# Kernel optimization log

Measured on AMD Instinct MI355X. Metric: run time of the kernel, lower is better.

The kernel has to match this reference:

```python
import jax, jax.numpy as jnp
import numpy as np

B, T, P, V, D, DINO, H, L = 32, 40, 256, 4096, 256, 384, 4, 2
HD = D // H          # head dim 64
DFF = 4 * D          # 1024
EPS = 1e-5


def setup_inputs() -> dict:
    key = jax.random.key(0)
    ks = iter(jax.random.split(key, 40))
    rn = lambda shape, s=0.02: jax.random.normal(next(ks), shape, jnp.float32) * s
    return dict(
        patches=jax.random.normal(next(ks), (B, P, DINO), jnp.float32),
        tokens=jax.random.randint(next(ks), (B, T), 0, V, jnp.int32),
        tok_emb=rn((V, D)),
        pos_emb=rn((1, T, D)),
        qkv_w=rn((L, 3 * D, D)), qkv_b=jnp.zeros((L, 3 * D), jnp.float32),
        out_w=rn((L, D, D)), out_b=jnp.zeros((L, D), jnp.float32),
        ln1_s=jnp.ones((L, D), jnp.float32), ln1_b=jnp.zeros((L, D), jnp.float32),
        w1=rn((L, DFF, D)), b1=jnp.zeros((L, DFF), jnp.float32),
        w2=rn((L, D, DFF)), b2=jnp.zeros((L, D), jnp.float32),
        ln2_s=jnp.ones((L, D), jnp.float32), ln2_b=jnp.zeros((L, D), jnp.float32),
        fus_w1=rn((D, DINO + D)), fus_b1=jnp.zeros((D,), jnp.float32),
        fus_w2=rn((D, D)), fus_b2=jnp.zeros((D,), jnp.float32),
        cls_w=rn((V, D)), cls_b=jnp.zeros((V,), jnp.float32),
    )


def _ln(x, s, b):
    m = jnp.mean(x, -1, keepdims=True)
    v = jnp.var(x, -1, keepdims=True)
    return (x - m) * jax.lax.rsqrt(v + EPS) * s + b


def _token_encoder(tokens, tok_emb, pos_emb, qkv_w, qkv_b, out_w, out_b,
                   ln1_s, ln1_b, w1, b1, w2, b2, ln2_s, ln2_b):
    # Causal full-sequence pass: output at position t equals re-running the
    # unmasked encoder on tokens[:, :t+1] and taking the last position.
    x = tok_emb[tokens] + pos_emb[:, :tokens.shape[1], :]   # [B,T,D]
    causal = jnp.triu(jnp.full((T, T), -1e9, jnp.float32), 1)  # [T,T]
    for l in range(L):  # fixed small layer count
        qkv = x @ qkv_w[l].T + qkv_b[l]                     # [B,T,3D]
        q, k, v = jnp.split(qkv, 3, axis=-1)
        q = q.reshape(B, T, H, HD).transpose(0, 2, 1, 3)    # [B,H,T,hd]
        k = k.reshape(B, T, H, HD).transpose(0, 2, 1, 3)
        v = v.reshape(B, T, H, HD).transpose(0, 2, 1, 3)
        scores = jnp.einsum('bhqd,bhkd->bhqk', q, k) / np.sqrt(HD).astype(np.float32)
        attn = jax.nn.softmax(scores + causal, axis=-1)
        ctx = jnp.einsum('bhqk,bhkd->bhqd', attn, v)        # [B,H,T,hd]
        ctx = ctx.transpose(0, 2, 1, 3).reshape(B, T, D)
        x = _ln(x + ctx @ out_w[l].T + out_b[l], ln1_s[l], ln1_b[l])
        h = jax.nn.relu(x @ w1[l].T + b1[l]) @ w2[l].T + b2[l]
        x = _ln(x + h, ln2_s[l], ln2_b[l])
    return x  # [B,T,D]


def reference(patches, tokens, tok_emb, pos_emb, qkv_w, qkv_b, out_w, out_b,
              ln1_s, ln1_b, w1, b1, w2, b2, ln2_s, ln2_b,
              fus_w1, fus_b1, fus_w2, fus_b2, cls_w, cls_b):
    enc = _token_encoder(tokens, tok_emb, pos_emb, qkv_w, qkv_b, out_w, out_b,
                         ln1_s, ln1_b, w1, b1, w2, b2, ln2_s, ln2_b)  # [B,T,D]
    # context for step 0 is zeros; step t>0 uses encoder output at position t-1
    ctx = jnp.concatenate([jnp.zeros((B, 1, D), enc.dtype), enc[:, :-1]], axis=1)  # [B,T,D]
    # fusion MLP: split the concat-linear into a patch part and a context part
    wp, wc = fus_w1[:, :DINO], fus_w1[:, DINO:]
    pproj = patches @ wp.T                                  # [B,P,D]
    cproj = ctx @ wc.T + fus_b1                             # [B,T,D]
    h = jax.nn.gelu(pproj[:, None, :, :] + cproj[:, :, None, :], approximate=False)  # [B,T,P,D]
    fused = h @ fus_w2.T + fus_b2                           # [B,T,P,D]
    # sigmoid+gather of the 4096-way logits == gather classifier rows, dot, sigmoid
    w_sel = cls_w[tokens]                                   # [B,T,D]
    b_sel = cls_b[tokens]                                   # [B,T]
    logits = jnp.einsum('btpd,btd->btp', fused, w_sel) + b_sel[:, :, None]
    probs = jax.nn.sigmoid(logits)                          # [B,T,P]
    return probs.transpose(0, 2, 1)                         # [B,P,T] == [B,256,40]
```

## Files before the change

kernel.cpp:

```cpp
#include <hip/hip_runtime.h>
#include <hip/hip_bf16.h>

#define B_ 32
#define T_ 40
#define P_ 256
#define V_ 4096
#define D_ 256
#define DINO_ 384
#define H_ 4
#define L_ 2
#define HD_ 64
#define DFF_ 1024
#define EPS_ 1e-5f

typedef __bf16 bf16;
typedef __bf16 bf16x8 __attribute__((ext_vector_type(8)));
typedef float f32x4 __attribute__((ext_vector_type(4)));

#define OFF_QKV 0
#define OFF_OUTW 393216
#define OFF_W1 524288
#define OFF_W2 1048576
#define OFF_FUS 1572864
#define WB_TOTAL 1736704
#define CONV_BLOCKS 848
#define PAT_BLOCKS 1536
#define PREP_UNITS 3728

__device__ __forceinline__ bf16x8 cvt8(const float* p) {
  float4 f0 = *(const float4*)p;
  float4 f1 = *(const float4*)(p + 4);
  bf16x8 v;
  v[0] = (bf16)f0.x; v[1] = (bf16)f0.y; v[2] = (bf16)f0.z; v[3] = (bf16)f0.w;
  v[4] = (bf16)f1.x; v[5] = (bf16)f1.y; v[6] = (bf16)f1.z; v[7] = (bf16)f1.w;
  return v;
}

struct GemmSM  { bf16 As[32 * 72];  bf16 Ws[32 * 72]; };
struct CprojSM { bf16 As[32 * 264]; bf16 Ws[32 * 72]; };
struct AttnSM  { float q[20][65]; float k[40][65]; float v[40][65]; float s[20][41]; };
struct PrepSM  { float tile[32][33]; };
struct FinalSM { float2 cws[4][D_]; };
struct RowSM   { bf16 As[32 * 72];  bf16 Ws[256 * 72]; };

struct Params {
  const float* patches; const int* tokens; const float* tok_emb; const float* pos_emb;
  const float* qkv_w; const float* qkv_b; const float* out_w; const float* out_b;
  const float* ln1_s; const float* ln1_b; const float* w1; const float* b1;
  const float* w2; const float* b2; const float* ln2_s; const float* ln2_b;
  const float* fus_w1; const float* fus_b1; const float* fus_w2; const float* fus_b2;
  const float* cls_w; const float* cls_b; float* out;
  float* x; float* qkvbuf; float* attbuf; float* s; float* pprojT; float* cw;
  bf16* wb; bf16* w2Tb; bf16* patb; bf16* hb;
};

template <int ABF16, int OBF16, int RELU, int RESID, int GATH, int CW>
__device__ __forceinline__ void tile_gemm(
    bf16* As, bf16* Ws, const void* Av, const bf16* W, const float* bias,
    const float* resid, const int* tokens, void* outv, int K, int lda,
    int ldw, int ldc, int bm, int bn) {
  const int tid = threadIdx.x;
  const int lane = tid & 63;
  const int wv = tid >> 6;
  const int mi = wv & 1, ni = wv >> 1;
  const int col = lane & 15, quad = lane >> 4;
  const int srow = tid >> 3, kc = (tid & 7) * 8;
  const float* Af = (const float*)Av;
  const bf16* Ab = (const bf16*)Av;
  const float* Ag = GATH ? (Af + (long)tokens[bm + srow] * D_) : nullptr;
  const bf16* Wp = W + (long)(bn + srow) * ldw + kc;

  f32x4 acc = {0.f, 0.f, 0.f, 0.f};
  for (int kk = 0; kk < K; kk += 64) {
    if (GATH)
      *(bf16x8*)&As[srow * 72 + kc] = cvt8(Ag + kk + kc);
    else if (ABF16)
      *(bf16x8*)&As[srow * 72 + kc] = *(const bf16x8*)(Ab + (long)(bm + srow) * lda + kk + kc);
    else
      *(bf16x8*)&As[srow * 72 + kc] = cvt8(Af + (long)(bm + srow) * lda + kk + kc);
    *(bf16x8*)&Ws[srow * 72 + kc] = *(const bf16x8*)(Wp + kk);
    __syncthreads();
#pragma unroll
    for (int ki = 0; ki < 2; ++ki) {
      bf16x8 afr = *(const bf16x8*)&As[(mi * 16 + col) * 72 + ki * 32 + quad * 8];
      bf16x8 bfr = *(const bf16x8*)&Ws[(ni * 16 + col) * 72 + ki * 32 + quad * 8];
      acc = __builtin_amdgcn_mfma_f32_16x16x32_bf16(afr, bfr, acc, 0, 0, 0);
    }
    __syncthreads();
  }
  const int n = bn + ni * 16 + col;
  float bv = bias ? bias[n] : 0.0f;
#pragma unroll
  for (int r = 0; r < 4; ++r) {
    int m = bm + mi * 16 + quad * 4 + r;
    float val = acc[r] + bv;
    if (RESID) val += resid[(long)m * D_ + n];
    if (RELU) val = fmaxf(val, 0.0f);
    if (CW == 1) ((float*)outv)[(long)m * (2 * D_) + n * 2] = val;
    else if (CW == 2) ((float*)outv)[(long)m * (2 * D_) + n * 2 + 1] = val;
    else if (OBF16) ((bf16*)outv)[(long)m * ldc + n] = (bf16)val;
    else ((float*)outv)[(long)m * ldc + n] = val;
  }
}

__device__ __forceinline__ void do_prep(PrepSM& ps, const Params& P, int u) {
  int tid = threadIdx.x;
  if (u < 1280) {
    P.x[u * D_ + tid] = P.tok_emb[(long)P.tokens[u] * D_ + tid] + P.pos_emb[(u % T_) * D_ + tid];
  } else if (u < 1344) {
    int tt = u - 1280;
    int bx = (tt & 7) * 32, by = (tt >> 3) * 32;
    int tx = tid & 31, ty = tid >> 5;
#pragma unroll
    for (int i = 0; i < 32; i += 8) ps.tile[ty + i][tx] = P.fus_w2[(by + ty + i) * D_ + bx + tx];
    __syncthreads();
#pragma unroll
    for (int i = 0; i < 32; i += 8)
      P.w2Tb[(bx + ty + i) * D_ + by + tx] = (bf16)ps.tile[tx][ty + i];
  } else if (u < 1344 + CONV_BLOCKS) {
    long f = (long)(u - 1344) * 2048 + tid * 8;
    const float* src; long off;
    if (f < OFF_OUTW)      { src = P.qkv_w;  off = f; }
    else if (f < OFF_W1)   { src = P.out_w;  off = f - OFF_OUTW; }
    else if (f < OFF_W2)   { src = P.w1;     off = f - OFF_W1; }
    else if (f < OFF_FUS)  { src = P.w2;     off = f - OFF_W2; }
    else                   { src = P.fus_w1; off = f - OFF_FUS; }
    *(bf16x8*)&P.wb[f] = cvt8(src + off);
  } else {
    long f = (long)(u - 1344 - CONV_BLOCKS) * 2048 + tid * 8;
    *(bf16x8*)&P.patb[f] = cvt8(P.patches + f);
  }
}

__device__ __forceinline__ void do_qkv(GemmSM& g, const Params& P, int l, int u) {
  tile_gemm<0, 0, 0, 0, 0, 0>(g.As, g.Ws, P.x, P.wb + OFF_QKV + (long)l * 3 * D_ * D_,
                              P.qkv_b + l * 3 * D_, nullptr, nullptr, P.qkvbuf,
                              256, D_, D_, 3 * D_, (u / 24) * 32, (u % 24) * 32);
}
__device__ __forceinline__ void do_w1(GemmSM& g, const Params& P, int l, int u) {
  tile_gemm<0, 1, 1, 0, 0, 0>(g.As, g.Ws, P.x, P.wb + OFF_W1 + (long)l * DFF_ * D_,
                              P.b1 + l * DFF_, nullptr, nullptr, P.hb,
                              256, D_, D_, DFF_, (u / 32) * 32, (u % 32) * 32);
}
__device__ __forceinline__ void do_w2(GemmSM& g, const Params& P, int l, int u) {
  tile_gemm<1, 0, 0, 1, 0, 0>(g.As, g.Ws, P.hb, P.wb + OFF_W2 + (long)l * D_ * DFF_,
                              P.b2 + l * D_, P.x, nullptr, P.s,
                              DFF_, DFF_, DFF_, D_, (u / 8) * 32, (u % 8) * 32);
}
__device__ __forceinline__ void do_pproj(GemmSM& g, const Params& P, int t) {
  int bn = (t & 7) * 32; int y = t >> 3; int bb = y >> 3; int bm = (y & 7) * 32;
  tile_gemm<1, 0, 0, 0, 0, 0>(g.As, g.Ws, P.wb + OFF_FUS, P.patb + (long)bb * P_ * DINO_,
                              nullptr, nullptr, nullptr, P.pprojT + (long)bb * D_ * P_,
                              384, 640, DINO_, P_, bm, bn);
}
__device__ __forceinline__ void do_weff(GemmSM& g, const Params& P, int t) {
  tile_gemm<0, 0, 0, 0, 1, 2>(g.As, g.Ws, P.cls_w, P.w2Tb, nullptr, nullptr,
                              P.tokens, P.cw, 256, D_, D_, D_,
                              (t / 8) * 32, (t % 8) * 32);
}

__device__ __forceinline__ void do_attn(AttnSM& A, const Params& P, int u) {
  int h = u & 3, b = (u >> 2) & 31, zq = u >> 7;
  int r0 = zq * 20;
  int tid = threadIdx.x;
  int lane = tid & 63, wv = tid >> 6;
  const float* qkv = P.qkvbuf;
  for (int idx = tid; idx < T_ * HD_; idx += 256) {
    int t = idx >> 6, d = idx & 63;
    long base = (long)(b * T_ + t) * (3 * D_) + h * HD_ + d;
    A.k[t][d] = qkv[base + D_];
    A.v[t][d] = qkv[base + 2 * D_];
    if (t < 20) A.q[t][d] = qkv[(long)(b * T_ + r0 + t) * (3 * D_) + h * HD_ + d];
  }
  __syncthreads();
  for (int idx = tid; idx < 20 * T_; idx += 256) {
    int i = idx / T_, j = idx - i * T_;
    if (j <= r0 + i) {
      float acc = 0.f;
#pragma unroll
      for (int d = 0; d < HD_; ++d) acc += A.q[i][d] * A.k[j][d];
      A.s[i][j] = acc * 0.125f;
    }
  }
  __syncthreads();
  for (int rr = wv; rr < 20; rr += 4) {
    int hi = r0 + rr;
    float val = (lane <= hi) ? A.s[rr][lane] : -1e30f;
    float mx = val;
#pragma unroll
    for (int mk = 1; mk < 64; mk <<= 1) mx = fmaxf(mx, __shfl_xor(mx, mk));
    float e = (lane <= hi)
                  ? __builtin_amdgcn_exp2f((val - mx) * 1.4426950408889634f)
                  : 0.f;
    float sum = e;
#pragma unroll
    for (int mk = 1; mk < 64; mk <<= 1) sum += __shfl_xor(sum, mk);
    float inv = __builtin_amdgcn_rcpf(sum);
    if (lane < T_) A.s[rr][lane] = e * inv;
  }
  __syncthreads();
  for (int idx = tid; idx < 20 * HD_; idx += 256) {
    int i = idx >> 6, d = idx & 63;
    int hi = r0 + i;
    float acc = 0.f;
    for (int j = 0; j <= hi; ++j) acc += A.s[i][j] * A.v[j][d];
    P.attbuf[(long)(b * T_ + hi) * D_ + h * HD_ + d] = acc;
  }
}

__device__ __forceinline__ void do_cproj(CprojSM& c, const Params& P, int bm, int bn) {
  const int tid = threadIdx.x;
  const int lane = tid & 63;
  const int wv = tid >> 6;
  const int mi = wv & 1, ni = wv >> 1;
  const int col = lane & 15, quad = lane >> 4;
  const int srow = tid >> 3, kc = (tid & 7) * 8;
  const int gm = bm + srow;
  f32x4 acc = {0.f, 0.f, 0.f, 0.f};
  const int cg = (tid & 7) * 32;
  const int t = gm % T_;
  if (t == 0) {
    bf16x8 z8 = {};
#pragma unroll
    for (int i = 0; i < 4; ++i) *(bf16x8*)&c.As[srow * 264 + cg + i * 8] = z8;
  } else {
    const float* sp = P.s + (long)(gm - 1) * D_ + cg;
    float v[32];
    float sum = 0.f, ss = 0.f;
#pragma unroll
    for (int i = 0; i < 8; ++i) {
      float4 f = *(const float4*)(sp + i * 4);
      v[i*4] = f.x; v[i*4+1] = f.y; v[i*4+2] = f.z; v[i*4+3] = f.w;
      sum += f.x + f.y + f.z + f.w;
      ss += f.x*f.x + f.y*f.y + f.z*f.z + f.w*f.w;
    }
#pragma unroll
    for (int mk = 1; mk < 8; mk <<= 1) {
      sum += __shfl_xor(sum, mk);
      ss += __shfl_xor(ss, mk);
    }
    float mean = sum * (1.0f / D_);
    float inv = rsqrtf(ss * (1.0f / D_) - mean * mean + EPS_);
    const float* lng = P.ln2_s + D_;
    const float* lnb = P.ln2_b + D_;
#pragma unroll
    for (int i = 0; i < 8; ++i) {
      float4 g4 = *(const float4*)(lng + cg + i * 4);
      float4 b4 = *(const float4*)(lnb + cg + i * 4);
      c.As[srow*264 + cg + i*4]     = (bf16)((v[i*4]   - mean) * inv * g4.x + b4.x);
      c.As[srow*264 + cg + i*4 + 1] = (bf16)((v[i*4+1] - mean) * inv * g4.y + b4.y);
      c.As[srow*264 + cg + i*4 + 2] = (bf16)((v[i*4+2] - mean) * inv * g4.z + b4.z);
      c.As[srow*264 + cg + i*4 + 3] = (bf16)((v[i*4+3] - mean) * inv * g4.w + b4.w);
    }
  }
  __syncthreads();
  const bf16* Wp = P.wb + OFF_FUS + 384 + (long)(bn + srow) * 640 + kc;
  for (int kk = 0; kk < 256; kk += 64) {
    *(bf16x8*)&c.Ws[srow * 72 + kc] = *(const bf16x8*)(Wp + kk);
    __syncthreads();
#pragma unroll
    for (int ki = 0; ki < 2; ++ki) {
      bf16x8 afr = *(const bf16x8*)&c.As[(mi*16 + col) * 264 + kk + ki*32 + quad*8];
      bf16x8 bfr = *(const bf16x8*)&c.Ws[(ni*16 + col) * 72 + ki*32 + quad*8];
      acc = __builtin_amdgcn_mfma_f32_16x16x32_bf16(afr, bfr, acc, 0, 0, 0);
    }
    __syncthreads();
  }
  const int n = bn + ni * 16 + col;
  float bv = P.fus_b1[n];
#pragma unroll
  for (int r = 0; r < 4; ++r) {
    int m = bm + mi * 16 + quad * 4 + r;
    P.cw[(long)m * (2 * D_) + n * 2] = acc[r] + bv;
  }
}

__device__ __forceinline__ void do_final(FinalSM& F, const Params& P, int u) {
  int tid = threadIdx.x;
  int lane = tid & 63, wv = tid >> 6;
  int px = u & 3, rest = u >> 2;
  int ty = rest % 10, b = rest / 10;
  int p = px * 64 + lane;
  int t = ty * 4 + wv;
  int mbase = b * T_ + ty * 4;
  for (int idx = tid; idx < 4 * D_; idx += 256) {
    int tt = idx >> 8, e = idx & 255;
    F.cws[tt][e] = ((const float2*)P.cw)[(long)(mbase + tt) * D_ + e];
  }
  __syncthreads();

  int m = b * T_ + t;
  int tok = P.tokens[m];
  const float* cr = P.cls_w + (long)tok * D_;
  float bacc = 0.f;
#pragma unroll
  for (int i = 0; i < 4; ++i) bacc += cr[lane + i * 64] * P.fus_b2[lane + i * 64];
#pragma unroll
  for (int mk = 1; mk < 64; mk <<= 1) bacc += __shfl_xor(bacc, mk);
  float beff = bacc + P.cls_b[tok];

  const float* ppb = P.pprojT + (long)b * (D_ * P_);
  float acc = 0.f;
#pragma unroll 8
  for (int e = 0; e < D_; ++e) {
    float pp = ppb[e * P_ + p];
    float2 c = F.cws[wv][e];
    float x = pp + c.x;
    float ex = __builtin_amdgcn_exp2f(-2.4554248f * x);
    float r = __builtin_amdgcn_rcpf(1.0f + ex);
    acc = fmaf(x * r, c.y, acc);
  }
  float logit = acc + beff;
  float es = __builtin_amdgcn_exp2f(-1.4426950408889634f * logit);
  P.out[(long)(b * P_ + p) * T_ + t] = __builtin_amdgcn_rcpf(1.0f + es);
}

template <int ABF16>
__global__ __launch_bounds__(256) void rowln_k(
    const void* __restrict__ Av, const bf16* __restrict__ W,
    const float* __restrict__ bias, const float* __restrict__ resid,
    const float* __restrict__ lng, const float* __restrict__ lnb,
    float* __restrict__ xout, int K, int lda, int ldw) {
  __shared__ RowSM sm;
  const int tid = threadIdx.x;
  const int lane = tid & 63;
  const int wv = tid >> 6;
  const int mi = wv & 1, nh = wv >> 1;
  const int col = lane & 15, quad = lane >> 4;
  const int srow = tid >> 3, kc = (tid & 7) * 8;
  const int bm = blockIdx.x * 32;
  const float* Af = (const float*)Av;
  const bf16* Ab = (const bf16*)Av;

  f32x4 acc[8];
#pragma unroll
  for (int i = 0; i < 8; ++i) acc[i] = (f32x4){0.f, 0.f, 0.f, 0.f};

  for (int kk = 0; kk < K; kk += 64) {
    if (ABF16)
      *(bf16x8*)&sm.As[srow * 72 + kc] =
          *(const bf16x8*)(Ab + (long)(bm + srow) * lda + kk + kc);
    else
      *(bf16x8*)&sm.As[srow * 72 + kc] = cvt8(Af + (long)(bm + srow) * lda + kk + kc);
    {
      const bf16* wp = W + (long)tid * ldw + kk;
#pragma unroll
      for (int j = 0; j < 8; ++j)
        *(bf16x8*)&sm.Ws[tid * 72 + j * 8] = *(const bf16x8*)(wp + j * 8);
    }
    __syncthreads();
#pragma unroll
    for (int nn = 0; nn < 8; ++nn) {
      const int ni = nh * 8 + nn;
#pragma unroll
      for (int ki = 0; ki < 2; ++ki) {
        bf16x8 afr = *(const bf16x8*)&sm.As[(mi * 16 + col) * 72 + ki * 32 + quad * 8];
        bf16x8 bfr = *(const bf16x8*)&sm.Ws[(ni * 16 + col) * 72 + ki * 32 + quad * 8];
        acc[nn] = __builtin_amdgcn_mfma_f32_16x16x32_bf16(afr, bfr, acc[nn], 0, 0, 0);
      }
    }
    __syncthreads();
  }

  float* S = (float*)sm.Ws;
#pragma unroll
  for (int nn = 0; nn < 8; ++nn) {
    const int n = (nh * 8 + nn) * 16 + col;
    const float bv = bias[n];
#pragma unroll
    for (int r = 0; r < 4; ++r) {
      const int m = mi * 16 + quad * 4 + r;
      S[m * 260 + n] = acc[nn][r] + bv + resid[(long)(bm + m) * D_ + n];
    }
  }
  __syncthreads();
  {
    const int row = tid >> 3, cg = (tid & 7) * 32;
    float v[32];
    float sum = 0.f, ss = 0.f;
#pragma unroll
    for (int i = 0; i < 8; ++i) {
      float4 f = *(const float4*)&S[row * 260 + cg + i * 4];
      v[i*4] = f.x; v[i*4+1] = f.y; v[i*4+2] = f.z; v[i*4+3] = f.w;
      sum += f.x + f.y + f.z + f.w;
      ss += f.x*f.x + f.y*f.y + f.z*f.z + f.w*f.w;
    }
#pragma unroll
    for (int mk = 1; mk < 8; mk <<= 1) {
      sum += __shfl_xor(sum, mk);
      ss += __shfl_xor(ss, mk);
    }
    const float mean = sum * (1.0f / D_);
    const float inv = rsqrtf(ss * (1.0f / D_) - mean * mean + EPS_);
#pragma unroll
    for (int i = 0; i < 8; ++i) {
      float4 g4 = *(const float4*)(lng + cg + i * 4);
      float4 b4 = *(const float4*)(lnb + cg + i * 4);
      float4 o;
      o.x = (v[i*4]   - mean) * inv * g4.x + b4.x;
      o.y = (v[i*4+1] - mean) * inv * g4.y + b4.y;
      o.z = (v[i*4+2] - mean) * inv * g4.z + b4.z;
      o.w = (v[i*4+3] - mean) * inv * g4.w + b4.w;
      *(float4*)(xout + (long)(bm + row) * D_ + cg + i * 4) = o;
    }
  }
}

__global__ __launch_bounds__(256) void prep_k(Params P) {
  __shared__ PrepSM ps; do_prep(ps, P, blockIdx.x);
}
__global__ __launch_bounds__(256) void qkv_k(Params P, int l) {
  __shared__ GemmSM g; do_qkv(g, P, l, blockIdx.x);
}
__global__ __launch_bounds__(256) void apw_k(Params P) {
  __shared__ union __align__(16) { AttnSM a; GemmSM g; } sm;
  int bid = blockIdx.x;
  if (bid < 256) do_attn(sm.a, P, bid);
  else if (bid < 2304) do_pproj(sm.g, P, bid - 256);
  else do_weff(sm.g, P, bid - 2304);
}
__global__ __launch_bounds__(256) void attn_k(Params P) {
  __shared__ AttnSM a; do_attn(a, P, blockIdx.x);
}
__global__ __launch_bounds__(256) void w1_k(Params P, int l) {
  __shared__ GemmSM g; do_w1(g, P, l, blockIdx.x);
}
__global__ __launch_bounds__(256) void w2_k(Params P, int l) {
  __shared__ GemmSM g; do_w2(g, P, l, blockIdx.x);
}
__global__ __launch_bounds__(256) void cproj_k(Params P) {
  __shared__ CprojSM c; do_cproj(c, P, blockIdx.y * 32, blockIdx.x * 32);
}
__global__ __launch_bounds__(256) void final_k(Params P) {
  __shared__ FinalSM f; do_final(f, P, blockIdx.x);
}

extern "C" void kernel_launch(void* const* d_in, const int* in_sizes, int n_in, void* d_out,
                              int out_size, void* d_ws, size_t ws_size, hipStream_t stream) {
  Params P;
  P.patches = (const float*)d_in[0];
  P.tokens = (const int*)d_in[1];
  P.tok_emb = (const float*)d_in[2];
  P.pos_emb = (const float*)d_in[3];
  P.qkv_w = (const float*)d_in[4];
  P.qkv_b = (const float*)d_in[5];
  P.out_w = (const float*)d_in[6];
  P.out_b = (const float*)d_in[7];
  P.ln1_s = (const float*)d_in[8];
  P.ln1_b = (const float*)d_in[9];
  P.w1 = (const float*)d_in[10];
  P.b1 = (const float*)d_in[11];
  P.w2 = (const float*)d_in[12];
  P.b2 = (const float*)d_in[13];
  P.ln2_s = (const float*)d_in[14];
  P.ln2_b = (const float*)d_in[15];
  P.fus_w1 = (const float*)d_in[16];
  P.fus_b1 = (const float*)d_in[17];
  P.fus_w2 = (const float*)d_in[18];
  P.fus_b2 = (const float*)d_in[19];
  P.cls_w = (const float*)d_in[20];
  P.cls_b = (const float*)d_in[21];
  P.out = (float*)d_out;

  const int MT = B_ * T_;
  P.x = (float*)d_ws;
  P.qkvbuf = P.x + MT * D_;
  P.attbuf = P.qkvbuf + MT * 3 * D_;
  P.s = P.attbuf + MT * D_;
  P.pprojT = P.s + MT * D_;
  P.cw = P.pprojT + (long)B_ * D_ * P_;
  P.wb = (bf16*)(P.cw + MT * D_ * 2);
  P.w2Tb = P.wb + WB_TOTAL;
  P.patb = P.w2Tb + D_ * D_;
  P.hb = P.patb + (long)B_ * P_ * DINO_;

  prep_k<<<PREP_UNITS, 256, 0, stream>>>(P);
  qkv_k<<<960, 256, 0, stream>>>(P, 0);
  apw_k<<<2624, 256, 0, stream>>>(P);
  rowln_k<0><<<40, 256, 0, stream>>>(P.attbuf, P.wb + OFF_OUTW, P.out_b, P.x,
                                     P.ln1_s, P.ln1_b, P.x, 256, 256, 256);
  w1_k<<<1280, 256, 0, stream>>>(P, 0);
  rowln_k<1><<<40, 256, 0, stream>>>(P.hb, P.wb + OFF_W2, P.b2, P.x,
                                     P.ln2_s, P.ln2_b, P.x, 1024, 1024, 1024);
  qkv_k<<<960, 256, 0, stream>>>(P, 1);
  attn_k<<<256, 256, 0, stream>>>(P);
  rowln_k<0><<<40, 256, 0, stream>>>(P.attbuf, P.wb + OFF_OUTW + D_ * D_,
                                     P.out_b + D_, P.x, P.ln1_s + D_,
                                     P.ln1_b + D_, P.x, 256, 256, 256);
  w1_k<<<1280, 256, 0, stream>>>(P, 1);
  w2_k<<<320, 256, 0, stream>>>(P, 1);
  cproj_k<<<dim3(8, 40), 256, 0, stream>>>(P);
  final_k<<<1280, 256, 0, stream>>>(P);
}
```

Before: 267.3 us.

## Fuse attention, out-proj+LN, and FFN+LN into one per-layer kernel

Replaces the separate attention, out-projection+LayerNorm, W1 and W2+LayerNorm launches with one layer kernel. Each of 80 blocks handles 16 rows end to end, keeping attention context, the hidden activations and the residual in shared memory. The pproj and weff work is split across the two layer kernels as extra blocks so it runs alongside the layer blocks. This removes several launches and global round-trips for the hidden activations. The cost is that only 80 blocks do the heavy FFN work, each streaming every layer weight, so parallelism is lower and weight traffic repeats across blocks.

```diff
diff --git a/kernel.cpp b/kernel.cpp
--- a/kernel.cpp
+++ b/kernel.cpp
@@ -38,10 +38,16 @@
 
 struct GemmSM  { bf16 As[32 * 72];  bf16 Ws[32 * 72]; };
 struct CprojSM { bf16 As[32 * 264]; bf16 Ws[32 * 72]; };
-struct AttnSM  { float q[20][65]; float k[40][65]; float v[40][65]; float s[20][41]; };
 struct PrepSM  { float tile[32][33]; };
 struct FinalSM { float2 cws[4][D_]; };
-struct RowSM   { bf16 As[32 * 72];  bf16 Ws[256 * 72]; };
+struct __align__(16) LayerSM {
+  bf16 CP[16 * 264];
+  union {
+    struct { float KS[80 * 68]; float VS[80 * 68]; float QS[16 * 68]; float SS[16 * 64]; } at;
+    struct { bf16 Ws[256 * 72]; float S1[16 * 260]; bf16 HB[16 * 136]; } gm;
+  } u;
+};
+union __align__(16) LayerU { LayerSM L; GemmSM g; };
 
 struct Params {
   const float* patches; const int* tokens; const float* tok_emb; const float* pos_emb;
@@ -137,16 +143,6 @@
                               P.qkv_b + l * 3 * D_, nullptr, nullptr, P.qkvbuf,
                               256, D_, D_, 3 * D_, (u / 24) * 32, (u % 24) * 32);
 }
-__device__ __forceinline__ void do_w1(GemmSM& g, const Params& P, int l, int u) {
-  tile_gemm<0, 1, 1, 0, 0, 0>(g.As, g.Ws, P.x, P.wb + OFF_W1 + (long)l * DFF_ * D_,
-                              P.b1 + l * DFF_, nullptr, nullptr, P.hb,
-                              256, D_, D_, DFF_, (u / 32) * 32, (u % 32) * 32);
-}
-__device__ __forceinline__ void do_w2(GemmSM& g, const Params& P, int l, int u) {
-  tile_gemm<1, 0, 0, 1, 0, 0>(g.As, g.Ws, P.hb, P.wb + OFF_W2 + (long)l * D_ * DFF_,
-                              P.b2 + l * D_, P.x, nullptr, P.s,
-                              DFF_, DFF_, DFF_, D_, (u / 8) * 32, (u % 8) * 32);
-}
 __device__ __forceinline__ void do_pproj(GemmSM& g, const Params& P, int t) {
   int bn = (t & 7) * 32; int y = t >> 3; int bb = y >> 3; int bm = (y & 7) * 32;
   tile_gemm<1, 0, 0, 0, 0, 0>(g.As, g.Ws, P.wb + OFF_FUS, P.patb + (long)bb * P_ * DINO_,
@@ -157,55 +153,6 @@
   tile_gemm<0, 0, 0, 0, 1, 2>(g.As, g.Ws, P.cls_w, P.w2Tb, nullptr, nullptr,
                               P.tokens, P.cw, 256, D_, D_, D_,
                               (t / 8) * 32, (t % 8) * 32);
-}
-
-__device__ __forceinline__ void do_attn(AttnSM& A, const Params& P, int u) {
-  int h = u & 3, b = (u >> 2) & 31, zq = u >> 7;
-  int r0 = zq * 20;
-  int tid = threadIdx.x;
-  int lane = tid & 63, wv = tid >> 6;
-  const float* qkv = P.qkvbuf;
-  for (int idx = tid; idx < T_ * HD_; idx += 256) {
-    int t = idx >> 6, d = idx & 63;
-    long base = (long)(b * T_ + t) * (3 * D_) + h * HD_ + d;
-    A.k[t][d] = qkv[base + D_];
-    A.v[t][d] = qkv[base + 2 * D_];
-    if (t < 20) A.q[t][d] = qkv[(long)(b * T_ + r0 + t) * (3 * D_) + h * HD_ + d];
-  }
-  __syncthreads();
-  for (int idx = tid; idx < 20 * T_; idx += 256) {
-    int i = idx / T_, j = idx - i * T_;
-    if (j <= r0 + i) {
-      float acc = 0.f;
-#pragma unroll
-      for (int d = 0; d < HD_; ++d) acc += A.q[i][d] * A.k[j][d];
-      A.s[i][j] = acc * 0.125f;
-    }
-  }
-  __syncthreads();
-  for (int rr = wv; rr < 20; rr += 4) {
-    int hi = r0 + rr;
-    float val = (lane <= hi) ? A.s[rr][lane] : -1e30f;
-    float mx = val;
-#pragma unroll
-    for (int mk = 1; mk < 64; mk <<= 1) mx = fmaxf(mx, __shfl_xor(mx, mk));
-    float e = (lane <= hi)
-                  ? __builtin_amdgcn_exp2f((val - mx) * 1.4426950408889634f)
-                  : 0.f;
-    float sum = e;
-#pragma unroll
-    for (int mk = 1; mk < 64; mk <<= 1) sum += __shfl_xor(sum, mk);
-    float inv = __builtin_amdgcn_rcpf(sum);
-    if (lane < T_) A.s[rr][lane] = e * inv;
-  }
-  __syncthreads();
-  for (int idx = tid; idx < 20 * HD_; idx += 256) {
-    int i = idx >> 6, d = idx & 63;
-    int hi = r0 + i;
-    float acc = 0.f;
-    for (int j = 0; j <= hi; ++j) acc += A.s[i][j] * A.v[j][d];
-    P.attbuf[(long)(b * T_ + hi) * D_ + h * HD_ + d] = acc;
-  }
 }
 
 __device__ __forceinline__ void do_cproj(CprojSM& c, const Params& P, int bm, int bn) {
@@ -315,93 +262,258 @@
   P.out[(long)(b * P_ + p) * T_ + t] = __builtin_amdgcn_rcpf(1.0f + es);
 }
 
-template <int ABF16>
-__global__ __launch_bounds__(256) void rowln_k(
-    const void* __restrict__ Av, const bf16* __restrict__ W,
-    const float* __restrict__ bias, const float* __restrict__ resid,
-    const float* __restrict__ lng, const float* __restrict__ lnb,
-    float* __restrict__ xout, int K, int lda, int ldw) {
-  __shared__ RowSM sm;
+template <int LAYER>
+__global__ __launch_bounds__(256) void layer_k(Params P) {
+  __shared__ LayerU sm;
+  const int bid = blockIdx.x;
+  if (bid >= 80) {
+    int t = bid - 80 + (LAYER == 0 ? 0 : 1024);
+    if (t < 2048) do_pproj(sm.g, P, t);
+    else do_weff(sm.g, P, t - 2048);
+    return;
+  }
   const int tid = threadIdx.x;
   const int lane = tid & 63;
   const int wv = tid >> 6;
-  const int mi = wv & 1, nh = wv >> 1;
   const int col = lane & 15, quad = lane >> 4;
-  const int srow = tid >> 3, kc = (tid & 7) * 8;
-  const int bm = blockIdx.x * 32;
-  const float* Af = (const float*)Av;
-  const bf16* Ab = (const bf16*)Av;
-
-  f32x4 acc[8];
-#pragma unroll
-  for (int i = 0; i < 8; ++i) acc[i] = (f32x4){0.f, 0.f, 0.f, 0.f};
-
-  for (int kk = 0; kk < K; kk += 64) {
-    if (ABF16)
-      *(bf16x8*)&sm.As[srow * 72 + kc] =
-          *(const bf16x8*)(Ab + (long)(bm + srow) * lda + kk + kc);
-    else
-      *(bf16x8*)&sm.As[srow * 72 + kc] = cvt8(Af + (long)(bm + srow) * lda + kk + kc);
-    {
-      const bf16* wp = W + (long)tid * ldw + kk;
-#pragma unroll
-      for (int j = 0; j < 8; ++j)
-        *(bf16x8*)&sm.Ws[tid * 72 + j * 8] = *(const bf16x8*)(wp + j * 8);
-    }
-    __syncthreads();
-#pragma unroll
-    for (int nn = 0; nn < 8; ++nn) {
-      const int ni = nh * 8 + nn;
+  const int R0 = bid * 16;
+  const int b_lo = R0 / T_, b_hi = (R0 + 15) / T_;
+  const int base = b_lo * T_, nr = (b_hi - b_lo + 1) * T_;
+
+  {
+    auto& A = sm.L.u.at;
+    for (int h = 0; h < H_; ++h) {
+      for (int idx = tid; idx < nr * 64; idx += 256) {
+        int t = idx >> 6, d = idx & 63;
+        long qb = (long)(base + t) * (3 * D_) + h * HD_ + d;
+        A.KS[t * 68 + d] = P.qkvbuf[qb + D_];
+        A.VS[t * 68 + d] = P.qkvbuf[qb + 2 * D_];
+      }
+      for (int idx = tid; idx < 16 * 64; idx += 256) {
+        int i = idx >> 6, d = idx & 63;
+        A.QS[i * 68 + d] = P.qkvbuf[(long)(R0 + i) * (3 * D_) + h * HD_ + d];
+      }
+      __syncthreads();
+      for (int idx = tid; idx < 16 * T_; idx += 256) {
+        int i = idx / T_, j = idx - i * T_;
+        int gr = R0 + i, ti = gr % T_;
+        if (j <= ti) {
+          int kr = (gr / T_) * T_ - base + j;
+          float acc = 0.f;
+#pragma unroll
+          for (int d = 0; d < 64; ++d) acc += A.QS[i * 68 + d] * A.KS[kr * 68 + d];
+          A.SS[i * 64 + j] = acc * 0.125f;
+        }
+      }
+      __syncthreads();
+      for (int rr = wv; rr < 16; rr += 4) {
+        int ti = (R0 + rr) % T_;
+        float val = (lane <= ti) ? A.SS[rr * 64 + lane] : -1e30f;
+        float mx = val;
+#pragma unroll
+        for (int mk = 1; mk < 64; mk <<= 1) mx = fmaxf(mx, __shfl_xor(mx, mk));
+        float e = (lane <= ti)
+                      ? __builtin_amdgcn_exp2f((val - mx) * 1.4426950408889634f)
+                      : 0.f;
+        float sum = e;
+#pragma unroll
+        for (int mk = 1; mk < 64; mk <<= 1) sum += __shfl_xor(sum, mk);
+        float inv = __builtin_amdgcn_rcpf(sum);
+        if (lane < T_) A.SS[rr * 64 + lane] = e * inv;
+      }
+      __syncthreads();
+      for (int idx = tid; idx < 16 * 64; idx += 256) {
+        int i = idx >> 6, d = idx & 63;
+        int gr = R0 + i, ti = gr % T_;
+        int koff = (gr / T_) * T_ - base;
+        float acc = 0.f;
+        for (int j = 0; j <= ti; ++j) acc += A.SS[i * 64 + j] * A.VS[(koff + j) * 68 + d];
+        sm.L.CP[i * 264 + h * HD_ + d] = (bf16)acc;
+      }
+      __syncthreads();
+    }
+  }
+
+  auto& G = sm.L.u.gm;
+  const bf16* Wout = P.wb + OFF_OUTW + (long)LAYER * D_ * D_;
+  f32x4 accp[4];
+#pragma unroll
+  for (int i = 0; i < 4; ++i) accp[i] = (f32x4){0.f, 0.f, 0.f, 0.f};
+  for (int kc = 0; kc < 4; ++kc) {
+    const bf16* wp = Wout + (long)tid * D_ + kc * 64;
+#pragma unroll
+    for (int j = 0; j < 8; ++j)
+      *(bf16x8*)&G.Ws[tid * 72 + j * 8] = *(const bf16x8*)(wp + j * 8);
+    __syncthreads();
+#pragma unroll
+    for (int t = 0; t < 4; ++t) {
+      int ni = wv * 4 + t;
 #pragma unroll
       for (int ki = 0; ki < 2; ++ki) {
-        bf16x8 afr = *(const bf16x8*)&sm.As[(mi * 16 + col) * 72 + ki * 32 + quad * 8];
-        bf16x8 bfr = *(const bf16x8*)&sm.Ws[(ni * 16 + col) * 72 + ki * 32 + quad * 8];
-        acc[nn] = __builtin_amdgcn_mfma_f32_16x16x32_bf16(afr, bfr, acc[nn], 0, 0, 0);
-      }
-    }
-    __syncthreads();
-  }
-
-  float* S = (float*)sm.Ws;
-#pragma unroll
-  for (int nn = 0; nn < 8; ++nn) {
-    const int n = (nh * 8 + nn) * 16 + col;
-    const float bv = bias[n];
-#pragma unroll
-    for (int r = 0; r < 4; ++r) {
-      const int m = mi * 16 + quad * 4 + r;
-      S[m * 260 + n] = acc[nn][r] + bv + resid[(long)(bm + m) * D_ + n];
+        bf16x8 afr = *(const bf16x8*)&sm.L.CP[col * 264 + kc * 64 + ki * 32 + quad * 8];
+        bf16x8 bfr = *(const bf16x8*)&G.Ws[(ni * 16 + col) * 72 + ki * 32 + quad * 8];
+        accp[t] = __builtin_amdgcn_mfma_f32_16x16x32_bf16(afr, bfr, accp[t], 0, 0, 0);
+      }
+    }
+    __syncthreads();
+  }
+  {
+    const float* outb = P.out_b + LAYER * D_;
+#pragma unroll
+    for (int t = 0; t < 4; ++t) {
+      int n = (wv * 4 + t) * 16 + col;
+#pragma unroll
+      for (int r = 0; r < 4; ++r) {
+        int m = quad * 4 + r;
+        G.S1[m * 260 + n] = accp[t][r] + outb[n] + P.x[(long)(R0 + m) * D_ + n];
+      }
     }
   }
   __syncthreads();
-  {
-    const int row = tid >> 3, cg = (tid & 7) * 32;
+
+  if (tid < 128) {
+    int row = tid >> 3, cg = (tid & 7) * 32;
     float v[32];
     float sum = 0.f, ss = 0.f;
 #pragma unroll
-    for (int i = 0; i < 8; ++i) {
-      float4 f = *(const float4*)&S[row * 260 + cg + i * 4];
-      v[i*4] = f.x; v[i*4+1] = f.y; v[i*4+2] = f.z; v[i*4+3] = f.w;
-      sum += f.x + f.y + f.z + f.w;
-      ss += f.x*f.x + f.y*f.y + f.z*f.z + f.w*f.w;
+    for (int i = 0; i < 32; ++i) {
+      float f = G.S1[row * 260 + cg + i];
+      v[i] = f; sum += f; ss += f * f;
     }
 #pragma unroll
     for (int mk = 1; mk < 8; mk <<= 1) {
       sum += __shfl_xor(sum, mk);
       ss += __shfl_xor(ss, mk);
     }
-    const float mean = sum * (1.0f / D_);
-    const float inv = rsqrtf(ss * (1.0f / D_) - mean * mean + EPS_);
-#pragma unroll
-    for (int i = 0; i < 8; ++i) {
-      float4 g4 = *(const float4*)(lng + cg + i * 4);
-      float4 b4 = *(const float4*)(lnb + cg + i * 4);
-      float4 o;
-      o.x = (v[i*4]   - mean) * inv * g4.x + b4.x;
-      o.y = (v[i*4+1] - mean) * inv * g4.y + b4.y;
-      o.z = (v[i*4+2] - mean) * inv * g4.z + b4.z;
-      o.w = (v[i*4+3] - mean) * inv * g4.w + b4.w;
-      *(float4*)(xout + (long)(bm + row) * D_ + cg + i * 4) = o;
+    float mean = sum * (1.0f / D_);
+    float inv = rsqrtf(ss * (1.0f / D_) - mean * mean + EPS_);
+    const float* lg = P.ln1_s + LAYER * D_;
+    const float* lb = P.ln1_b + LAYER * D_;
+#pragma unroll
+    for (int i = 0; i < 32; ++i) {
+      float o = (v[i] - mean) * inv * lg[cg + i] + lb[cg + i];
+      G.S1[row * 260 + cg + i] = o;
+      sm.L.CP[row * 264 + cg + i] = (bf16)o;
+    }
+  }
+  __syncthreads();
+
+  const bf16* W1 = P.wb + OFF_W1 + (long)LAYER * DFF_ * D_;
+  const bf16* W2 = P.wb + OFF_W2 + (long)LAYER * D_ * DFF_;
+  const float* b1l = P.b1 + LAYER * DFF_;
+  f32x4 acc2[4];
+#pragma unroll
+  for (int i = 0; i < 4; ++i) acc2[i] = (f32x4){0.f, 0.f, 0.f, 0.f};
+  for (int kk2 = 0; kk2 < 8; ++kk2) {
+    f32x4 acch[2];
+    acch[0] = (f32x4){0.f, 0.f, 0.f, 0.f};
+    acch[1] = (f32x4){0.f, 0.f, 0.f, 0.f};
+    for (int kc = 0; kc < 4; ++kc) {
+      const bf16* wp = W1 + (long)(kk2 * 128 + (tid >> 1)) * D_ + kc * 64 + (tid & 1) * 32;
+#pragma unroll
+      for (int j = 0; j < 4; ++j)
+        *(bf16x8*)&G.Ws[(tid >> 1) * 72 + (tid & 1) * 32 + j * 8] = *(const bf16x8*)(wp + j * 8);
+      __syncthreads();
+#pragma unroll
+      for (int t2 = 0; t2 < 2; ++t2) {
+        int ni = wv * 2 + t2;
+#pragma unroll
+        for (int ki = 0; ki < 2; ++ki) {
+          bf16x8 afr = *(const bf16x8*)&sm.L.CP[col * 264 + kc * 64 + ki * 32 + quad * 8];
+          bf16x8 bfr = *(const bf16x8*)&G.Ws[(ni * 16 + col) * 72 + ki * 32 + quad * 8];
+          acch[t2] = __builtin_amdgcn_mfma_f32_16x16x32_bf16(afr, bfr, acch[t2], 0, 0, 0);
+        }
+      }
+      __syncthreads();
+    }
+#pragma unroll
+    for (int t2 = 0; t2 < 2; ++t2) {
+      int n2 = (wv * 2 + t2) * 16 + col;
+#pragma unroll
+      for (int r = 0; r < 4; ++r) {
+        int m = quad * 4 + r;
+        float hv = fmaxf(acch[t2][r] + b1l[kk2 * 128 + n2], 0.f);
+        G.HB[m * 136 + n2] = (bf16)hv;
+      }
+    }
+    __syncthreads();
+    for (int sc = 0; sc < 2; ++sc) {
+      const bf16* wp = W2 + (long)tid * DFF_ + kk2 * 128 + sc * 64;
+#pragma unroll
+      for (int j = 0; j < 8; ++j)
+        *(bf16x8*)&G.Ws[tid * 72 + j * 8] = *(const bf16x8*)(wp + j * 8);
+      __syncthreads();
+#pragma unroll
+      for (int t = 0; t < 4; ++t) {
+        int ni = wv * 4 + t;
+#pragma unroll
+        for (int ki = 0; ki < 2; ++ki) {
+          bf16x8 afr = *(const bf16x8*)&G.HB[col * 136 + sc * 64 + ki * 32 + quad * 8];
+          bf16x8 bfr = *(const bf16x8*)&G.Ws[(ni * 16 + col) * 72 + ki * 32 + quad * 8];
+          acc2[t] = __builtin_amdgcn_mfma_f32_16x16x32_bf16(afr, bfr, acc2[t], 0, 0, 0);
+        }
+      }
+      __syncthreads();
+    }
+  }
+
+  {
+    const float* b2l = P.b2 + LAYER * D_;
+    float vals[4][4];
+#pragma unroll
+    for (int t = 0; t < 4; ++t) {
+      int n = (wv * 4 + t) * 16 + col;
+#pragma unroll
+      for (int r = 0; r < 4; ++r) {
+        int m = quad * 4 + r;
+        vals[t][r] = acc2[t][r] + b2l[n] + G.S1[m * 260 + n];
+      }
+    }
+    if (LAYER == 1) {
+#pragma unroll
+      for (int t = 0; t < 4; ++t) {
+        int n = (wv * 4 + t) * 16 + col;
+#pragma unroll
+        for (int r = 0; r < 4; ++r) {
+          int m = quad * 4 + r;
+          P.s[(long)(R0 + m) * D_ + n] = vals[t][r];
+        }
+      }
+    } else {
+#pragma unroll
+      for (int t = 0; t < 4; ++t) {
+        int n = (wv * 4 + t) * 16 + col;
+#pragma unroll
+        for (int r = 0; r < 4; ++r) {
+          int m = quad * 4 + r;
+          G.S1[m * 260 + n] = vals[t][r];
+        }
+      }
+      __syncthreads();
+      if (tid < 128) {
+        int row = tid >> 3, cg = (tid & 7) * 32;
+        float v[32];
+        float sum = 0.f, ss = 0.f;
+#pragma unroll
+        for (int i = 0; i < 32; ++i) {
+          float f = G.S1[row * 260 + cg + i];
+          v[i] = f; sum += f; ss += f * f;
+        }
+#pragma unroll
+        for (int mk = 1; mk < 8; mk <<= 1) {
+          sum += __shfl_xor(sum, mk);
+          ss += __shfl_xor(ss, mk);
+        }
+        float mean = sum * (1.0f / D_);
+        float inv = rsqrtf(ss * (1.0f / D_) - mean * mean + EPS_);
+        const float* lg = P.ln2_s;
+        const float* lb = P.ln2_b;
+#pragma unroll
+        for (int i = 0; i < 32; ++i) {
+          float o = (v[i] - mean) * inv * lg[cg + i] + lb[cg + i];
+          P.x[(long)(R0 + row) * D_ + cg + i] = o;
+        }
+      }
     }
   }
 }
@@ -412,24 +524,8 @@
 __global__ __launch_bounds__(256) void qkv_k(Params P, int l) {
   __shared__ GemmSM g; do_qkv(g, P, l, blockIdx.x);
 }
-__global__ __launch_bounds__(256) void apw_k(Params P) {
-  __shared__ union __align__(16) { AttnSM a; GemmSM g; } sm;
-  int bid = blockIdx.x;
-  if (bid < 256) do_attn(sm.a, P, bid);
-  else if (bid < 2304) do_pproj(sm.g, P, bid - 256);
-  else do_weff(sm.g, P, bid - 2304);
-}
-__global__ __launch_bounds__(256) void attn_k(Params P) {
-  __shared__ AttnSM a; do_attn(a, P, blockIdx.x);
-}
-__global__ __launch_bounds__(256) void w1_k(Params P, int l) {
-  __shared__ GemmSM g; do_w1(g, P, l, blockIdx.x);
-}
-__global__ __launch_bounds__(256) void w2_k(Params P, int l) {
-  __shared__ GemmSM g; do_w2(g, P, l, blockIdx.x);
-}
 __global__ __launch_bounds__(256) void cproj_k(Params P) {
-  __shared__ CprojSM c; do_cproj(c, P, blockIdx.y * 32, blockIdx.x * 32);
+  __shared__ CprojSM c; do_cproj(c, P, (blockIdx.x >> 3) * 32, (blockIdx.x & 7) * 32);
 }
 __global__ __launch_bounds__(256) void final_k(Params P) {
   __shared__ FinalSM f; do_final(f, P, blockIdx.x);
@@ -476,19 +572,9 @@
 
   prep_k<<<PREP_UNITS, 256, 0, stream>>>(P);
   qkv_k<<<960, 256, 0, stream>>>(P, 0);
-  apw_k<<<2624, 256, 0, stream>>>(P);
-  rowln_k<0><<<40, 256, 0, stream>>>(P.attbuf, P.wb + OFF_OUTW, P.out_b, P.x,
-                                     P.ln1_s, P.ln1_b, P.x, 256, 256, 256);
-  w1_k<<<1280, 256, 0, stream>>>(P, 0);
-  rowln_k<1><<<40, 256, 0, stream>>>(P.hb, P.wb + OFF_W2, P.b2, P.x,
-                                     P.ln2_s, P.ln2_b, P.x, 1024, 1024, 1024);
+  layer_k<0><<<80 + 1024, 256, 0, stream>>>(P);
   qkv_k<<<960, 256, 0, stream>>>(P, 1);
-  attn_k<<<256, 256, 0, stream>>>(P);
-  rowln_k<0><<<40, 256, 0, stream>>>(P.attbuf, P.wb + OFF_OUTW + D_ * D_,
-                                     P.out_b + D_, P.x, P.ln1_s + D_,
-                                     P.ln1_b + D_, P.x, 256, 256, 256);
-  w1_k<<<1280, 256, 0, stream>>>(P, 1);
-  w2_k<<<320, 256, 0, stream>>>(P, 1);
-  cproj_k<<<dim3(8, 40), 256, 0, stream>>>(P);
+  layer_k<1><<<80 + 1024 + 320, 256, 0, stream>>>(P);
+  cproj_k<<<320, 256, 0, stream>>>(P);
   final_k<<<1280, 256, 0, stream>>>(P);
 }
```

After: 343.8 us. 1.29x slower.

## Read fp32 weights directly in GEMMs and split fused row-LN into GEMM plus LN

Applied to the files above, without the earlier changes.

The prep kernel no longer converts the encoder weights (qkv, out, w1, w2) to bf16. The GEMM tile loader now converts fp32 weights on the fly, which removes a full pre-pass over about 1.5M weights. The fused 40-block row GEMM+LayerNorm kernels are replaced by a 320-block tiled projection GEMM that writes a residual sum, followed by a separate warp-per-row LayerNorm kernel. This gives more parallelism at the cost of extra launches and a round trip through global memory. The w2 GEMM of layer 0 is also restored as its own launch.

```diff
diff --git a/kernel.cpp b/kernel.cpp
--- a/kernel.cpp
+++ b/kernel.cpp
@@ -17,15 +17,10 @@
 typedef __bf16 bf16x8 __attribute__((ext_vector_type(8)));
 typedef float f32x4 __attribute__((ext_vector_type(4)));
 
-#define OFF_QKV 0
-#define OFF_OUTW 393216
-#define OFF_W1 524288
-#define OFF_W2 1048576
-#define OFF_FUS 1572864
-#define WB_TOTAL 1736704
-#define CONV_BLOCKS 848
+#define FUS_ELEMS 163840
+#define FUS_BLOCKS 80
 #define PAT_BLOCKS 1536
-#define PREP_UNITS 3728
+#define PREP_UNITS 2960
 
 __device__ __forceinline__ bf16x8 cvt8(const float* p) {
   float4 f0 = *(const float4*)p;
@@ -41,7 +36,6 @@
 struct AttnSM  { float q[20][65]; float k[40][65]; float v[40][65]; float s[20][41]; };
 struct PrepSM  { float tile[32][33]; };
 struct FinalSM { float2 cws[4][D_]; };
-struct RowSM   { bf16 As[32 * 72];  bf16 Ws[256 * 72]; };
 
 struct Params {
   const float* patches; const int* tokens; const float* tok_emb; const float* pos_emb;
@@ -54,9 +48,9 @@
   bf16* wb; bf16* w2Tb; bf16* patb; bf16* hb;
 };
 
-template <int ABF16, int OBF16, int RELU, int RESID, int GATH, int CW>
+template <int ABF16, int WF32, int OBF16, int RELU, int RESID, int GATH, int CW>
 __device__ __forceinline__ void tile_gemm(
-    bf16* As, bf16* Ws, const void* Av, const bf16* W, const float* bias,
+    bf16* As, bf16* Ws, const void* Av, const void* Wv, const float* bias,
     const float* resid, const int* tokens, void* outv, int K, int lda,
     int ldw, int ldc, int bm, int bn) {
   const int tid = threadIdx.x;
@@ -68,7 +62,8 @@
   const float* Af = (const float*)Av;
   const bf16* Ab = (const bf16*)Av;
   const float* Ag = GATH ? (Af + (long)tokens[bm + srow] * D_) : nullptr;
-  const bf16* Wp = W + (long)(bn + srow) * ldw + kc;
+  const float* Wpf = (const float*)Wv + (long)(bn + srow) * ldw + kc;
+  const bf16* Wpb = (const bf16*)Wv + (long)(bn + srow) * ldw + kc;
 
   f32x4 acc = {0.f, 0.f, 0.f, 0.f};
   for (int kk = 0; kk < K; kk += 64) {
@@ -78,7 +73,10 @@
       *(bf16x8*)&As[srow * 72 + kc] = *(const bf16x8*)(Ab + (long)(bm + srow) * lda + kk + kc);
     else
       *(bf16x8*)&As[srow * 72 + kc] = cvt8(Af + (long)(bm + srow) * lda + kk + kc);
-    *(bf16x8*)&Ws[srow * 72 + kc] = *(const bf16x8*)(Wp + kk);
+    if (WF32)
+      *(bf16x8*)&Ws[srow * 72 + kc] = cvt8(Wpf + kk);
+    else
+      *(bf16x8*)&Ws[srow * 72 + kc] = *(const bf16x8*)(Wpb + kk);
     __syncthreads();
 #pragma unroll
     for (int ki = 0; ki < 2; ++ki) {
@@ -117,46 +115,45 @@
 #pragma unroll
     for (int i = 0; i < 32; i += 8)
       P.w2Tb[(bx + ty + i) * D_ + by + tx] = (bf16)ps.tile[tx][ty + i];
-  } else if (u < 1344 + CONV_BLOCKS) {
+  } else if (u < 1344 + FUS_BLOCKS) {
     long f = (long)(u - 1344) * 2048 + tid * 8;
-    const float* src; long off;
-    if (f < OFF_OUTW)      { src = P.qkv_w;  off = f; }
-    else if (f < OFF_W1)   { src = P.out_w;  off = f - OFF_OUTW; }
-    else if (f < OFF_W2)   { src = P.w1;     off = f - OFF_W1; }
-    else if (f < OFF_FUS)  { src = P.w2;     off = f - OFF_W2; }
-    else                   { src = P.fus_w1; off = f - OFF_FUS; }
-    *(bf16x8*)&P.wb[f] = cvt8(src + off);
+    *(bf16x8*)&P.wb[f] = cvt8(P.fus_w1 + f);
   } else {
-    long f = (long)(u - 1344 - CONV_BLOCKS) * 2048 + tid * 8;
+    long f = (long)(u - 1344 - FUS_BLOCKS) * 2048 + tid * 8;
     *(bf16x8*)&P.patb[f] = cvt8(P.patches + f);
   }
 }
 
 __device__ __forceinline__ void do_qkv(GemmSM& g, const Params& P, int l, int u) {
-  tile_gemm<0, 0, 0, 0, 0, 0>(g.As, g.Ws, P.x, P.wb + OFF_QKV + (long)l * 3 * D_ * D_,
-                              P.qkv_b + l * 3 * D_, nullptr, nullptr, P.qkvbuf,
-                              256, D_, D_, 3 * D_, (u / 24) * 32, (u % 24) * 32);
+  tile_gemm<0, 1, 0, 0, 0, 0, 0>(g.As, g.Ws, P.x, P.qkv_w + (long)l * 3 * D_ * D_,
+                                 P.qkv_b + l * 3 * D_, nullptr, nullptr, P.qkvbuf,
+                                 256, D_, D_, 3 * D_, (u / 24) * 32, (u % 24) * 32);
+}
+__device__ __forceinline__ void do_proj(GemmSM& g, const Params& P, int l, int u) {
+  tile_gemm<0, 1, 0, 0, 1, 0, 0>(g.As, g.Ws, P.attbuf, P.out_w + (long)l * D_ * D_,
+                                 P.out_b + l * D_, P.x, nullptr, P.s,
+                                 256, D_, D_, D_, (u / 8) * 32, (u % 8) * 32);
 }
 __device__ __forceinline__ void do_w1(GemmSM& g, const Params& P, int l, int u) {
-  tile_gemm<0, 1, 1, 0, 0, 0>(g.As, g.Ws, P.x, P.wb + OFF_W1 + (long)l * DFF_ * D_,
-                              P.b1 + l * DFF_, nullptr, nullptr, P.hb,
-                              256, D_, D_, DFF_, (u / 32) * 32, (u % 32) * 32);
+  tile_gemm<0, 1, 1, 1, 0, 0, 0>(g.As, g.Ws, P.x, P.w1 + (long)l * DFF_ * D_,
+                                 P.b1 + l * DFF_, nullptr, nullptr, P.hb,
+                                 256, D_, D_, DFF_, (u / 32) * 32, (u % 32) * 32);
 }
 __device__ __forceinline__ void do_w2(GemmSM& g, const Params& P, int l, int u) {
-  tile_gemm<1, 0, 0, 1, 0, 0>(g.As, g.Ws, P.hb, P.wb + OFF_W2 + (long)l * D_ * DFF_,
-                              P.b2 + l * D_, P.x, nullptr, P.s,
-                              DFF_, DFF_, DFF_, D_, (u / 8) * 32, (u % 8) * 32);
+  tile_gemm<1, 1, 0, 0, 1, 0, 0>(g.As, g.Ws, P.hb, P.w2 + (long)l * D_ * DFF_,
+                                 P.b2 + l * D_, P.x, nullptr, P.s,
+                                 DFF_, DFF_, DFF_, D_, (u / 8) * 32, (u % 8) * 32);
 }
 __device__ __forceinline__ void do_pproj(GemmSM& g, const Params& P, int t) {
   int bn = (t & 7) * 32; int y = t >> 3; int bb = y >> 3; int bm = (y & 7) * 32;
-  tile_gemm<1, 0, 0, 0, 0, 0>(g.As, g.Ws, P.wb + OFF_FUS, P.patb + (long)bb * P_ * DINO_,
-                              nullptr, nullptr, nullptr, P.pprojT + (long)bb * D_ * P_,
-                              384, 640, DINO_, P_, bm, bn);
+  tile_gemm<1, 0, 0, 0, 0, 0, 0>(g.As, g.Ws, P.wb, P.patb + (long)bb * P_ * DINO_,
+                                 nullptr, nullptr, nullptr, P.pprojT + (long)bb * D_ * P_,
+                                 384, 640, DINO_, P_, bm, bn);
 }
 __device__ __forceinline__ void do_weff(GemmSM& g, const Params& P, int t) {
-  tile_gemm<0, 0, 0, 0, 1, 2>(g.As, g.Ws, P.cls_w, P.w2Tb, nullptr, nullptr,
-                              P.tokens, P.cw, 256, D_, D_, D_,
-                              (t / 8) * 32, (t % 8) * 32);
+  tile_gemm<0, 0, 0, 0, 0, 1, 2>(g.As, g.Ws, P.cls_w, P.w2Tb, nullptr, nullptr,
+                                 P.tokens, P.cw, 256, D_, D_, D_,
+                                 (t / 8) * 32, (t % 8) * 32);
 }
 
 __device__ __forceinline__ void do_attn(AttnSM& A, const Params& P, int u) {
@@ -254,7 +251,7 @@
     }
   }
   __syncthreads();
-  const bf16* Wp = P.wb + OFF_FUS + 384 + (long)(bn + srow) * 640 + kc;
+  const bf16* Wp = P.wb + 384 + (long)(bn + srow) * 640 + kc;
   for (int kk = 0; kk < 256; kk += 64) {
     *(bf16x8*)&c.Ws[srow * 72 + kc] = *(const bf16x8*)(Wp + kk);
     __syncthreads();
@@ -315,97 +312,6 @@
   P.out[(long)(b * P_ + p) * T_ + t] = __builtin_amdgcn_rcpf(1.0f + es);
 }
 
-template <int ABF16>
-__global__ __launch_bounds__(256) void rowln_k(
-    const void* __restrict__ Av, const bf16* __restrict__ W,
-    const float* __restrict__ bias, const float* __restrict__ resid,
-    const float* __restrict__ lng, const float* __restrict__ lnb,
-    float* __restrict__ xout, int K, int lda, int ldw) {
-  __shared__ RowSM sm;
-  const int tid = threadIdx.x;
-  const int lane = tid & 63;
-  const int wv = tid >> 6;
-  const int mi = wv & 1, nh = wv >> 1;
-  const int col = lane & 15, quad = lane >> 4;
-  const int srow = tid >> 3, kc = (tid & 7) * 8;
-  const int bm = blockIdx.x * 32;
-  const float* Af = (const float*)Av;
-  const bf16* Ab = (const bf16*)Av;
-
-  f32x4 acc[8];
-#pragma unroll
-  for (int i = 0; i < 8; ++i) acc[i] = (f32x4){0.f, 0.f, 0.f, 0.f};
-
-  for (int kk = 0; kk < K; kk += 64) {
-    if (ABF16)
-      *(bf16x8*)&sm.As[srow * 72 + kc] =
-          *(const bf16x8*)(Ab + (long)(bm + srow) * lda + kk + kc);
-    else
-      *(bf16x8*)&sm.As[srow * 72 + kc] = cvt8(Af + (long)(bm + srow) * lda + kk + kc);
-    {
-      const bf16* wp = W + (long)tid * ldw + kk;
-#pragma unroll
-      for (int j = 0; j < 8; ++j)
-        *(bf16x8*)&sm.Ws[tid * 72 + j * 8] = *(const bf16x8*)(wp + j * 8);
-    }
-    __syncthreads();
-#pragma unroll
-    for (int nn = 0; nn < 8; ++nn) {
-      const int ni = nh * 8 + nn;
-#pragma unroll
-      for (int ki = 0; ki < 2; ++ki) {
-        bf16x8 afr = *(const bf16x8*)&sm.As[(mi * 16 + col) * 72 + ki * 32 + quad * 8];
-        bf16x8 bfr = *(const bf16x8*)&sm.Ws[(ni * 16 + col) * 72 + ki * 32 + quad * 8];
-        acc[nn] = __builtin_amdgcn_mfma_f32_16x16x32_bf16(afr, bfr, acc[nn], 0, 0, 0);
-      }
-    }
-    __syncthreads();
-  }
-
-  float* S = (float*)sm.Ws;
-#pragma unroll
-  for (int nn = 0; nn < 8; ++nn) {
-    const int n = (nh * 8 + nn) * 16 + col;
-    const float bv = bias[n];
-#pragma unroll
-    for (int r = 0; r < 4; ++r) {
-      const int m = mi * 16 + quad * 4 + r;
-      S[m * 260 + n] = acc[nn][r] + bv + resid[(long)(bm + m) * D_ + n];
-    }
-  }
-  __syncthreads();
-  {
-    const int row = tid >> 3, cg = (tid & 7) * 32;
-    float v[32];
-    float sum = 0.f, ss = 0.f;
-#pragma unroll
-    for (int i = 0; i < 8; ++i) {
-      float4 f = *(const float4*)&S[row * 260 + cg + i * 4];
-      v[i*4] = f.x; v[i*4+1] = f.y; v[i*4+2] = f.z; v[i*4+3] = f.w;
-      sum += f.x + f.y + f.z + f.w;
-      ss += f.x*f.x + f.y*f.y + f.z*f.z + f.w*f.w;
-    }
-#pragma unroll
-    for (int mk = 1; mk < 8; mk <<= 1) {
-      sum += __shfl_xor(sum, mk);
-      ss += __shfl_xor(ss, mk);
-    }
-    const float mean = sum * (1.0f / D_);
-    const float inv = rsqrtf(ss * (1.0f / D_) - mean * mean + EPS_);
-#pragma unroll
-    for (int i = 0; i < 8; ++i) {
-      float4 g4 = *(const float4*)(lng + cg + i * 4);
-      float4 b4 = *(const float4*)(lnb + cg + i * 4);
-      float4 o;
-      o.x = (v[i*4]   - mean) * inv * g4.x + b4.x;
-      o.y = (v[i*4+1] - mean) * inv * g4.y + b4.y;
-      o.z = (v[i*4+2] - mean) * inv * g4.z + b4.z;
-      o.w = (v[i*4+3] - mean) * inv * g4.w + b4.w;
-      *(float4*)(xout + (long)(bm + row) * D_ + cg + i * 4) = o;
-    }
-  }
-}
-
 __global__ __launch_bounds__(256) void prep_k(Params P) {
   __shared__ PrepSM ps; do_prep(ps, P, blockIdx.x);
 }
@@ -422,6 +328,34 @@
 __global__ __launch_bounds__(256) void attn_k(Params P) {
   __shared__ AttnSM a; do_attn(a, P, blockIdx.x);
 }
+__global__ __launch_bounds__(256) void proj_k(Params P, int l) {
+  __shared__ GemmSM g; do_proj(g, P, l, blockIdx.x);
+}
+__global__ __launch_bounds__(256) void ln_k(const float* __restrict__ s,
+                                            float* __restrict__ xout,
+                                            const float* __restrict__ g,
+                                            const float* __restrict__ be) {
+  int wv = threadIdx.x >> 6, lane = threadIdx.x & 63;
+  int m = blockIdx.x * 4 + wv;
+  float4 v = *(const float4*)(s + (long)m * D_ + lane * 4);
+  float sum = v.x + v.y + v.z + v.w;
+  float ss = v.x * v.x + v.y * v.y + v.z * v.z + v.w * v.w;
+#pragma unroll
+  for (int mk = 1; mk < 64; mk <<= 1) {
+    sum += __shfl_xor(sum, mk);
+    ss += __shfl_xor(ss, mk);
+  }
+  float mean = sum * (1.0f / D_);
+  float inv = rsqrtf(ss * (1.0f / D_) - mean * mean + EPS_);
+  float4 g4 = *(const float4*)(g + lane * 4);
+  float4 b4 = *(const float4*)(be + lane * 4);
+  float4 o;
+  o.x = (v.x - mean) * inv * g4.x + b4.x;
+  o.y = (v.y - mean) * inv * g4.y + b4.y;
+  o.z = (v.z - mean) * inv * g4.z + b4.z;
+  o.w = (v.w - mean) * inv * g4.w + b4.w;
+  *(float4*)(xout + (long)m * D_ + lane * 4) = o;
+}
 __global__ __launch_bounds__(256) void w1_k(Params P, int l) {
   __shared__ GemmSM g; do_w1(g, P, l, blockIdx.x);
 }
@@ -429,7 +363,7 @@
   __shared__ GemmSM g; do_w2(g, P, l, blockIdx.x);
 }
 __global__ __launch_bounds__(256) void cproj_k(Params P) {
-  __shared__ CprojSM c; do_cproj(c, P, blockIdx.y * 32, blockIdx.x * 32);
+  __shared__ CprojSM c; do_cproj(c, P, (blockIdx.x >> 3) * 32, (blockIdx.x & 7) * 32);
 }
 __global__ __launch_bounds__(256) void final_k(Params P) {
   __shared__ FinalSM f; do_final(f, P, blockIdx.x);
@@ -470,25 +404,24 @@
   P.pprojT = P.s + MT * D_;
   P.cw = P.pprojT + (long)B_ * D_ * P_;
   P.wb = (bf16*)(P.cw + MT * D_ * 2);
-  P.w2Tb = P.wb + WB_TOTAL;
+  P.w2Tb = P.wb + FUS_ELEMS;
   P.patb = P.w2Tb + D_ * D_;
   P.hb = P.patb + (long)B_ * P_ * DINO_;
 
   prep_k<<<PREP_UNITS, 256, 0, stream>>>(P);
   qkv_k<<<960, 256, 0, stream>>>(P, 0);
   apw_k<<<2624, 256, 0, stream>>>(P);
-  rowln_k<0><<<40, 256, 0, stream>>>(P.attbuf, P.wb + OFF_OUTW, P.out_b, P.x,
-                                     P.ln1_s, P.ln1_b, P.x, 256, 256, 256);
+  proj_k<<<320, 256, 0, stream>>>(P, 0);
+  ln_k<<<320, 256, 0, stream>>>(P.s, P.x, P.ln1_s, P.ln1_b);
   w1_k<<<1280, 256, 0, stream>>>(P, 0);
-  rowln_k<1><<<40, 256, 0, stream>>>(P.hb, P.wb + OFF_W2, P.b2, P.x,
-                                     P.ln2_s, P.ln2_b, P.x, 1024, 1024, 1024);
+  w2_k<<<320, 256, 0, stream>>>(P, 0);
+  ln_k<<<320, 256, 0, stream>>>(P.s, P.x, P.ln2_s, P.ln2_b);
   qkv_k<<<960, 256, 0, stream>>>(P, 1);
   attn_k<<<256, 256, 0, stream>>>(P);
-  rowln_k<0><<<40, 256, 0, stream>>>(P.attbuf, P.wb + OFF_OUTW + D_ * D_,
-                                     P.out_b + D_, P.x, P.ln1_s + D_,
-                                     P.ln1_b + D_, P.x, 256, 256, 256);
+  proj_k<<<320, 256, 0, stream>>>(P, 1);
+  ln_k<<<320, 256, 0, stream>>>(P.s, P.x, P.ln1_s + D_, P.ln1_b + D_);
   w1_k<<<1280, 256, 0, stream>>>(P, 1);
   w2_k<<<320, 256, 0, stream>>>(P, 1);
-  cproj_k<<<dim3(8, 40), 256, 0, stream>>>(P);
+  cproj_k<<<320, 256, 0, stream>>>(P);
   final_k<<<1280, 256, 0, stream>>>(P);
 }
```

Result: faster. 249.6 us (median of 3 runs) (-6.6%).
